# Kernel tuning notes

Hardware: AMD Instinct MI355X
Metric: run time of the kernel (lower is better)

The kernel has to match this reference:

```python
import jax, jax.numpy as jnp
import numpy as np
from jax import lax

V, E, T, F, K = 100000, 300, 50, 100, 3
B, S = 32, 512


def setup_inputs() -> dict:
    key = jax.random.key(0)
    ks = jax.random.split(key, 10)
    inp = {
        "x": jax.random.randint(ks[0], (B, S), 0, V),
        "tags": jax.random.randint(ks[1], (B, S), 0, T),
        "emb": jax.random.normal(ks[2], (V, E), dtype=jnp.float32),
        "conv_w": jax.random.normal(ks[3], (F, E, K), dtype=jnp.float32) / np.sqrt(E * K),
        "conv_b": jnp.zeros((F,), dtype=jnp.float32),
        "fc_w": jax.random.normal(ks[4], (T, F), dtype=jnp.float32) / np.sqrt(F),
        "fc_b": jnp.zeros((T,), dtype=jnp.float32),
        "start_trans": jax.random.uniform(ks[5], (T,), dtype=jnp.float32, minval=-0.1, maxval=0.1),
        "end_trans": jax.random.uniform(ks[6], (T,), dtype=jnp.float32, minval=-0.1, maxval=0.1),
        "trans": jax.random.uniform(ks[7], (T, T), dtype=jnp.float32, minval=-0.1, maxval=0.1),
    }
    return inp


def _emissions(x, emb, conv_w, conv_b, fc_w, fc_b):
    e = emb[x]                                   # [B,S,E] embedding gather
    e = jnp.transpose(e, (0, 2, 1))              # [B,E,S]
    h = lax.conv_general_dilated(e, conv_w, (1,), [(K // 2, K // 2)])  # [B,F,S] (NCW/OIW)
    h = jax.nn.relu(h + conv_b[None, :, None])   # dropout is identity in eval
    feat = jnp.transpose(h, (0, 2, 1))           # [B,S,F]
    return (jnp.einsum("bsf,tf->bst", feat, fc_w) + fc_b).astype(jnp.float32)  # [B,S,T]


def _crf_nll(emissions, tags, start_trans, end_trans, trans):
    # numerator: score of the gold tag path (full mask)
    em_tag = jnp.take_along_axis(emissions, tags[..., None], axis=-1)[..., 0]  # [B,S]
    num = (start_trans[tags[:, 0]]
           + em_tag.sum(-1)
           + trans[tags[:, :-1], tags[:, 1:]].sum(-1)
           + end_trans[tags[:, -1]])                                           # [B]

    # denominator: forward algorithm via scan over time
    alpha0 = start_trans[None, :] + emissions[:, 0]                             # [B,T]

    def step(alpha, em_t):
        # alpha: [B,T] prev scores; em_t: [B,T] emissions at t
        new = jax.nn.logsumexp(alpha[:, :, None] + trans[None] + em_t[:, None, :], axis=1)
        return new, None

    alpha, _ = lax.scan(step, alpha0, jnp.transpose(emissions[:, 1:], (1, 0, 2)))
    log_z = jax.nn.logsumexp(alpha + end_trans[None, :], axis=-1)               # [B]
    return -(num - log_z).sum()  # torchcrf default reduction='sum'; model returns -llh


def reference(x, tags, emb, conv_w, conv_b, fc_w, fc_b, start_trans, end_trans, trans):
    emissions = _emissions(x, emb, conv_w, conv_b, fc_w, fc_b)
    return _crf_nll(emissions, tags, start_trans, end_trans, trans)
```

## Files before the change

### kernel.cpp

```cpp
#include <hip/hip_runtime.h>
#include <hip/hip_bf16.h>
#include <math.h>

#define BB 32
#define SS 512
#define EE 300
#define FF 100
#define TT 50
#define CH 16
#define NC 32

typedef __attribute__((ext_vector_type(8))) short v8s;
typedef __attribute__((ext_vector_type(4))) float v4f;
#define MFMA16 __builtin_amdgcn_mfma_f32_16x16x32_bf16

#define AP 328
#define NCH 10
#define CKS 3
#define CHB (128 * 96)
#define A2P 136
#define MP 72

__device__ inline unsigned short f2bf(float v) {
    unsigned u = __float_as_uint(v);
    unsigned r = u + 0x7fff + ((u >> 16) & 1);
    return (unsigned short)(r >> 16);
}
__device__ inline float bf2f(short s) {
    return __uint_as_float(((unsigned)(unsigned short)s) << 16);
}
__device__ inline unsigned pkbf2(float a, float b) {
    __hip_bfloat162 h = __float22bfloat162_rn(make_float2(a, b));
    return *(unsigned*)&h;
}
__device__ inline v8s ldsld8(const short* p) {
    return *(const v8s*)__builtin_assume_aligned(p, 16);
}
__device__ inline void g2lds16(const void* g, void* l) {
    __builtin_amdgcn_global_load_lds(
        (const __attribute__((address_space(1))) unsigned int*)g,
        (__attribute__((address_space(3))) unsigned int*)l, 16, 0, 0);
}

__global__ void prep_kernel(const float* __restrict__ tr, const float* __restrict__ cw,
                            const float* __restrict__ fcw,
                            unsigned short* __restrict__ wB2,
                            unsigned short* __restrict__ fcwT2,
                            unsigned short* __restrict__ AT,
                            unsigned short* __restrict__ Ab,
                            float* __restrict__ accum, unsigned* __restrict__ cnt,
                            float* __restrict__ nllpart, unsigned* __restrict__ doneb)
{
    const int gid = blockIdx.x * 256 + threadIdx.x;
    const int gs  = 64 * 256;
    if (gid == 0) { *accum = 0.f; *cnt = 0u; }
    if (gid < BB) { nllpart[gid] = 0.f; doneb[gid] = 0u; }
    for (int idx = gid; idx < NCH * CKS * 8 * 512; idx += gs) {
        int e = idx & 7, p = (idx >> 3) & 63, blk = idx >> 9;
        int ch = blk / 24, rem = blk - ch * 24;
        int sl = rem >> 3, ft = rem & 7;
        int col = p >> 2, q = p & 3;
        int n  = ft * 16 + col;
        int gk = ch * 96 + sl * 32 + q * 8 + e;
        int kk = gk / 320, ee = gk - kk * 320;
        float v = (n < FF && ee < EE) ? cw[n * 900 + ee * 3 + kk] : 0.f;
        wB2[idx] = f2bf(v);
    }
    for (int idx = gid; idx < 16 * 512; idx += gs) {
        int e = idx & 7, p = (idx >> 3) & 63, blk = idx >> 9;
        int ks = blk >> 2, nt = blk & 3;
        int col = p >> 2, q = p & 3;
        int t = nt * 16 + col, f = ks * 32 + q * 8 + e;
        float v = (t < TT && f < FF) ? fcw[t * FF + f] : 0.f;
        fcwT2[idx] = f2bf(v);
    }
    for (int idx = gid; idx < 64 * 64; idx += gs) {
        int r = idx >> 6, c2 = idx & 63;
        AT[idx] = (r < TT && c2 < TT) ? f2bf(__expf(tr[c2 * TT + r])) : 0;
        Ab[idx] = (r < TT && c2 < TT) ? f2bf(__expf(tr[r * TT + c2])) : 0;
    }
}

__global__ __launch_bounds__(256, 3) void emis_kernel(
    const int* __restrict__ x, const float* __restrict__ emb,
    const unsigned short* __restrict__ wB2, const float* __restrict__ cb,
    const unsigned short* __restrict__ fcwT2, const float* __restrict__ fcb,
    const int* __restrict__ tags, const float* __restrict__ tr,
    const float* __restrict__ start, const float* __restrict__ endt,
    float* __restrict__ expem, float* __restrict__ nllpart)
{
    __shared__ __align__(16) short ldsA[34 * AP];
    __shared__ __align__(16) short ldsB[CHB];
    __shared__ float redN[2];

    const int b    = blockIdx.y;
    const int s0   = blockIdx.x * 32;
    const int tid  = threadIdx.x;
    const int wv   = tid >> 6;
    const int lane = tid & 63;
    const int col  = lane & 15;
    const int q    = lane >> 4;
    const int bofs = ((col << 2) | q) << 3;

#pragma unroll
    for (int it = 0; it < 6; ++it) {
        int seg = it * 4 + wv;
        g2lds16((const char*)wB2 + seg * 1024 + lane * 16,
                (char*)ldsB + seg * 1024);
    }

    int   xr[10], ofs[10], e0a[10];
#pragma unroll
    for (int it = 0; it < 10; ++it) {
        int g = tid + it * 256;
        int r = g / 75, eg = g - r * 75;
        int e0 = eg * 4;
        int src = s0 - 1 + r;
        bool v = (g < 2550) && (src >= 0) && (src < SS);
        xr[it]  = v ? x[b * SS + src] : -1;
        ofs[it] = r * AP + e0;
        e0a[it] = e0;
    }
    float4 vv[10];
#pragma unroll
    for (int it = 0; it < 10; ++it)
        vv[it] = (xr[it] >= 0)
               ? *(const float4*)(emb + (size_t)xr[it] * EE + e0a[it])
               : make_float4(0.f, 0.f, 0.f, 0.f);
#pragma unroll
    for (int it = 0; it < 10; ++it) {
        int g = tid + it * 256;
        if (g < 2550) {
            unsigned lo = pkbf2(vv[it].x, vv[it].y);
            unsigned hi = pkbf2(vv[it].z, vv[it].w);
            *(uint2*)&ldsA[ofs[it]] = make_uint2(lo, hi);
        }
    }
    if (tid < 34 * 5) {
        int r = tid / 5, c0 = 300 + (tid % 5) * 4;
        *(short4*)&ldsA[r * AP + c0] = make_short4(0, 0, 0, 0);
    }

    v4f acc[2][2];
#pragma unroll
    for (int a = 0; a < 2; ++a)
#pragma unroll
        for (int f = 0; f < 2; ++f) acc[a][f] = (v4f){0.f, 0.f, 0.f, 0.f};

    const int ftA = wv * 2, ftB = wv * 2 + 1;
    for (int ch = 0; ch < NCH; ++ch) {
        __syncthreads();
#pragma unroll
        for (int sl = 0; sl < CKS; ++sl) {
            int gk = ch * 96 + sl * 32;
            int kk = (gk >= 640) ? 2 : (gk >= 320 ? 1 : 0);
            int e0 = gk - kk * 320;
            v8s a0 = ldsld8(&ldsA[(col + kk) * AP + e0 + q * 8]);
            v8s a1 = ldsld8(&ldsA[(16 + col + kk) * AP + e0 + q * 8]);
            v8s b0 = ldsld8(&ldsB[((sl * 8 + ftA) << 9) + bofs]);
            v8s b1 = ldsld8(&ldsB[((sl * 8 + ftB) << 9) + bofs]);
            acc[0][0] = MFMA16(a0, b0, acc[0][0], 0, 0, 0);
            acc[0][1] = MFMA16(a0, b1, acc[0][1], 0, 0, 0);
            acc[1][0] = MFMA16(a1, b0, acc[1][0], 0, 0, 0);
            acc[1][1] = MFMA16(a1, b1, acc[1][1], 0, 0, 0);
        }
        __syncthreads();
        if (ch < NCH - 1) {
            const char* g = (const char*)(wB2 + (size_t)(ch + 1) * CHB);
#pragma unroll
            for (int it = 0; it < 6; ++it) {
                int seg = it * 4 + wv;
                g2lds16(g + seg * 1024 + lane * 16, (char*)ldsB + seg * 1024);
            }
        }
    }

    short* A2 = ldsA;
    short* B2 = ldsB;
#pragma unroll
    for (int it = 0; it < 4; ++it) {
        int seg = it * 4 + wv;
        g2lds16((const char*)fcwT2 + seg * 1024 + lane * 16,
                (char*)B2 + seg * 1024);
    }
#pragma unroll
    for (int st = 0; st < 2; ++st)
#pragma unroll
        for (int fi = 0; fi < 2; ++fi) {
            int f = (wv * 2 + fi) * 16 + col;
            float bias = (f < FF) ? cb[f] : 0.f;
#pragma unroll
            for (int rg = 0; rg < 4; ++rg) {
                int s = st * 16 + q * 4 + rg;
                float v = (f < FF) ? fmaxf(acc[st][fi][rg] + bias, 0.f) : 0.f;
                A2[s * A2P + f] = (short)f2bf(v);
            }
        }
    __syncthreads();

    if (wv < 2) {
        v4f a2[4];
#pragma unroll
        for (int nt = 0; nt < 4; ++nt) a2[nt] = (v4f){0.f, 0.f, 0.f, 0.f};
#pragma unroll
        for (int ks = 0; ks < 4; ++ks) {
            v8s af = ldsld8(&A2[(wv * 16 + col) * A2P + ks * 32 + q * 8]);
#pragma unroll
            for (int nt = 0; nt < 4; ++nt) {
                v8s bt = ldsld8(&B2[((ks * 4 + nt) << 9) + bofs]);
                a2[nt] = MFMA16(af, bt, a2[nt], 0, 0, 0);
            }
        }
        float fb0 = fcb[col], fb1 = fcb[16 + col], fb2 = fcb[32 + col];
        float fb3 = (col < 2) ? fcb[48 + col] : 0.f;
        float nllp = 0.f;
#pragma unroll
        for (int rg = 0; rg < 4; ++rg) {
            int s = s0 + wv * 16 + q * 4 + rg;
            float e0v = a2[0][rg] + fb0;
            float e1v = a2[1][rg] + fb1;
            float e2v = a2[2][rg] + fb2;
            float e3v = (col < 2) ? a2[3][rg] + fb3 : -1e30f;
            float m = fmaxf(fmaxf(e0v, e1v), fmaxf(e2v, e3v));
#pragma unroll
            for (int off = 1; off < 16; off <<= 1) m = fmaxf(m, __shfl_xor(m, off));
            int gidx = b * SS + s;
            int tg = tags[gidx];
            float* orow = expem + (size_t)gidx * TT;
            orow[col]      = __expf(e0v - m);
            orow[16 + col] = __expf(e1v - m);
            orow[32 + col] = __expf(e2v - m);
            if (col < 2) orow[48 + col] = __expf(e3v - m);
            if (tg == col)            nllp -= e0v;
            else if (tg == 16 + col)  nllp -= e1v;
            else if (tg == 32 + col)  nllp -= e2v;
            else if (col < 2 && tg == 48 + col) nllp -= e3v;
            if (col == 0) {
                nllp += m;
                if (s < SS - 1) nllp -= tr[tg * TT + tags[gidx + 1]];
                if (s == 0)      nllp -= start[tg];
                if (s == SS - 1) nllp -= endt[tg];
            }
        }
#pragma unroll
        for (int off = 1; off < 64; off <<= 1) nllp += __shfl_xor(nllp, off);
        if (lane == 0) redN[wv] = nllp;
    }
    __syncthreads();
    if (tid == 0) atomicAdd(nllpart + b, redN[0] + redN[1]);
}

__global__ __launch_bounds__(128) void chunkchain_kernel(
    const float* __restrict__ expem, const unsigned short* __restrict__ AT,
    const unsigned short* __restrict__ Ab,
    unsigned short* __restrict__ R, float* __restrict__ lsR,
    const float* __restrict__ start, const float* __restrict__ endt,
    const float* __restrict__ nllpart, unsigned* __restrict__ doneb,
    float* __restrict__ accum, unsigned* __restrict__ cnt,
    float* __restrict__ out)
{
    __shared__ __align__(16) short L[2][64 * MP];
    __shared__ __align__(16) float emL[CH][64];
    __shared__ float mxsh[2];
    __shared__ unsigned lastf;
    const int c = blockIdx.x, b = blockIdx.y;
    const int tid  = threadIdx.x;
    const int wv   = tid >> 6;
    const int lane = tid & 63;
    const int col = lane & 15, q = lane >> 4;
    const int t0 = c * CH + 1;
    const int nf = (c == NC - 1) ? (SS - 1 - (NC - 1) * CH) : CH;

    for (int idx = tid; idx < CH * 64; idx += 128) {
        int k = idx >> 6, m = idx & 63;
        float v = 0.f;
        if (m < TT && k < nf) v = expem[((size_t)(b * SS + t0 + k)) * TT + m];
        emL[k][m] = v;
    }

    v8s af[2][2];
#pragma unroll
    for (int jl = 0; jl < 2; ++jl)
#pragma unroll
        for (int kc = 0; kc < 2; ++kc)
            af[jl][kc] = *(const v8s*)(AT + ((wv * 2 + jl) * 16 + col) * 64 + kc * 32 + q * 8);
    __syncthreads();

    {
        const int row = tid >> 1, half = tid & 1;
        const v8s* arow = (const v8s*)(Ab + row * 64);
#pragma unroll
        for (int gh = 0; gh < 4; ++gh) {
            int g = half * 4 + gh;
            v8s a = arow[g];
            float f[8];
#pragma unroll
            for (int e = 0; e < 8; ++e) f[e] = bf2f(a[e]) * emL[0][g * 8 + e];
            uint4 o = make_uint4(pkbf2(f[0], f[1]), pkbf2(f[2], f[3]),
                                 pkbf2(f[4], f[5]), pkbf2(f[6], f[7]));
            *(uint4*)&L[0][row * MP + g * 8] = o;
        }
    }

    int cur = 0;
    for (int k = 1; k < nf; ++k) {
        __syncthreads();
        v8s bf[4][2];
#pragma unroll
        for (int nt = 0; nt < 4; ++nt)
#pragma unroll
            for (int kc = 0; kc < 2; ++kc)
                bf[nt][kc] = ldsld8(&L[cur][(nt * 16 + col) * MP + kc * 32 + q * 8]);
        v4f acc[2][4];
#pragma unroll
        for (int jl = 0; jl < 2; ++jl)
#pragma unroll
            for (int nt = 0; nt < 4; ++nt) {
                acc[jl][nt] = (v4f){0.f, 0.f, 0.f, 0.f};
                acc[jl][nt] = MFMA16(af[jl][0], bf[nt][0], acc[jl][nt], 0, 0, 0);
                acc[jl][nt] = MFMA16(af[jl][1], bf[nt][1], acc[jl][nt], 0, 0, 0);
            }
        if (k < nf - 1) {
#pragma unroll
            for (int jl = 0; jl < 2; ++jl) {
                const int jt = wv * 2 + jl;
                const float4 em4 = *(const float4*)&emL[k][jt * 16 + q * 4];
#pragma unroll
                for (int nt = 0; nt < 4; ++nt) {
                    uint2 o = make_uint2(
                        pkbf2(acc[jl][nt][0] * em4.x, acc[jl][nt][1] * em4.y),
                        pkbf2(acc[jl][nt][2] * em4.z, acc[jl][nt][3] * em4.w));
                    *(uint2*)&L[cur ^ 1][(nt * 16 + col) * MP + jt * 16 + q * 4] = o;
                }
            }
            cur ^= 1;
        } else {
            float vals[2][4][4];
            float mx = 0.f;
#pragma unroll
            for (int jl = 0; jl < 2; ++jl) {
                const int jt = wv * 2 + jl;
                const float4 em4 = *(const float4*)&emL[k][jt * 16 + q * 4];
#pragma unroll
                for (int nt = 0; nt < 4; ++nt) {
                    vals[jl][nt][0] = acc[jl][nt][0] * em4.x;
                    vals[jl][nt][1] = acc[jl][nt][1] * em4.y;
                    vals[jl][nt][2] = acc[jl][nt][2] * em4.z;
                    vals[jl][nt][3] = acc[jl][nt][3] * em4.w;
#pragma unroll
                    for (int r = 0; r < 4; ++r) mx = fmaxf(mx, vals[jl][nt][r]);
                }
            }
#pragma unroll
            for (int off = 1; off < 64; off <<= 1) mx = fmaxf(mx, __shfl_xor(mx, off));
            if (lane == 0) mxsh[wv] = mx;
            __syncthreads();
            mx = fmaxf(fmaxf(mxsh[0], mxsh[1]), 1e-37f);
            float inv = 1.f / mx;
            unsigned short* Rc = R + ((size_t)(b * NC + c) << 12);
#pragma unroll
            for (int jl = 0; jl < 2; ++jl)
#pragma unroll
                for (int nt = 0; nt < 4; ++nt)
#pragma unroll
                    for (int r = 0; r < 4; ++r)
                        Rc[((wv * 2 + jl) * 16 + q * 4 + r) * 64 + nt * 16 + col] =
                            f2bf(vals[jl][nt][r] * inv);
            if (tid == 0) lsR[b * NC + c] = __logf(mx);
        }
    }

    __syncthreads();
    if (tid == 0) {
        __threadfence();
        unsigned o = atomicAdd(doneb + b, 1u);
        lastf = (o == NC - 1) ? 1u : 0u;
    }
    __syncthreads();
    if (!lastf || wv != 0) return;

    __threadfence();
    const int i = lane;
    float* pvec = &emL[0][0];
    pvec[i] = (i < TT) ? __expf(start[i]) * expem[((size_t)(b * SS)) * TT + i] : 0.f;
    const unsigned short* Rb = R + ((size_t)(b * NC) << 12);
    v8s rb[4][8];
#pragma unroll
    for (int pc = 0; pc < 4; ++pc)
#pragma unroll
        for (int g = 0; g < 8; ++g)
            rb[pc][g] = *(const v8s*)(Rb + ((size_t)pc << 12) + i * 64 + g * 8);
    float logacc = 0.f;
#pragma unroll
    for (int cc = 0; cc < NC; ++cc) {
        const int slot = cc & 3;
        const float4* pv4 = (const float4*)pvec;
        float a0 = 0.f, a1 = 0.f, a2 = 0.f, a3 = 0.f;
#pragma unroll
        for (int g = 0; g < 8; ++g) {
            v8s v = rb[slot][g];
            float4 pA = pv4[g * 2], pB = pv4[g * 2 + 1];
            float* aa = (g & 3) == 0 ? &a0 : (g & 3) == 1 ? &a1 : (g & 3) == 2 ? &a2 : &a3;
            float t = *aa;
            t = fmaf(bf2f(v[0]), pA.x, t);
            t = fmaf(bf2f(v[1]), pA.y, t);
            t = fmaf(bf2f(v[2]), pA.z, t);
            t = fmaf(bf2f(v[3]), pA.w, t);
            t = fmaf(bf2f(v[4]), pB.x, t);
            t = fmaf(bf2f(v[5]), pB.y, t);
            t = fmaf(bf2f(v[6]), pB.z, t);
            t = fmaf(bf2f(v[7]), pB.w, t);
            *aa = t;
        }
        float acc2 = (a0 + a1) + (a2 + a3);
        if (cc + 4 < NC) {
            const unsigned short* Rn = Rb + ((size_t)(cc + 4) << 12);
#pragma unroll
            for (int g = 0; g < 8; ++g)
                rb[slot][g] = *(const v8s*)(Rn + i * 64 + g * 8);
        }
        float mx = acc2;
#pragma unroll
        for (int off = 1; off < 64; off <<= 1) mx = fmaxf(mx, __shfl_xor(mx, off));
        mx = fmaxf(mx, 1e-37f);
        logacc += __logf(mx) + lsR[b * NC + cc];
        pvec[i] = acc2 * (1.f / mx);
    }
    float sv = (i < TT) ? pvec[i] * __expf(endt[i]) : 0.f;
#pragma unroll
    for (int off = 1; off < 64; off <<= 1) sv += __shfl_xor(sv, off);
    if (i == 0) {
        float nll = nllpart[b] + logacc + __logf(sv);
        atomicAdd(accum, nll);
        __threadfence();
        unsigned o = atomicAdd(cnt, 1u);
        if (o == BB - 1) out[0] = atomicAdd(accum, 0.f);
    }
}

extern "C" void kernel_launch(void* const* d_in, const int* in_sizes, int n_in,
                              void* d_out, int out_size, void* d_ws, size_t ws_size,
                              hipStream_t stream)
{
    const int*   x    = (const int*)d_in[0];
    const int*   tags = (const int*)d_in[1];
    const float* emb  = (const float*)d_in[2];
    const float* cw   = (const float*)d_in[3];
    const float* cb   = (const float*)d_in[4];
    const float* fcw  = (const float*)d_in[5];
    const float* fcb  = (const float*)d_in[6];
    const float* st   = (const float*)d_in[7];
    const float* en   = (const float*)d_in[8];
    const float* tr   = (const float*)d_in[9];

    unsigned short* wB2   = (unsigned short*)d_ws;
    unsigned short* fcwT2 = wB2 + NCH * CKS * 8 * 512;
    unsigned short* ATm   = fcwT2 + 16 * 512;
    unsigned short* Abm   = ATm + 4096;
    unsigned short* Rm    = Abm + 4096;
    float* fbase   = (float*)(Rm + (size_t)BB * NC * 4096);
    float* expem   = fbase;
    float* lsR     = expem + (size_t)BB * SS * TT;
    float* nllpart = lsR + BB * NC;
    float* accum   = nllpart + BB;
    unsigned* cnt  = (unsigned*)(accum + 1);
    unsigned* doneb = cnt + 1;

    prep_kernel<<<dim3(64), 256, 0, stream>>>(tr, cw, fcw, wB2, fcwT2, ATm, Abm,
                                              accum, cnt, nllpart, doneb);
    emis_kernel<<<dim3(16, BB), 256, 0, stream>>>(x, emb, wB2, cb, fcwT2, fcb,
                                                  tags, tr, st, en, expem, nllpart);
    chunkchain_kernel<<<dim3(NC, BB), 128, 0, stream>>>(expem, ATm, Abm, Rm, lsR,
                                                        st, en, nllpart, doneb,
                                                        accum, cnt, (float*)d_out);
}
```

Baseline: 283.6 us.

## Replace sequential chunk matrix chain with parallel tree reduction across eight waves

The per-chunk product of 16 transfer matrices was computed by two waves stepping sequentially through time. Now eight waves each form a pair product in parallel (identity padding for short chunks), followed by a log-depth tree of LDS matrix products. This shortens the serial dependency chain within each block, but each wave does more MFMA work, the block grows to 512 threads, and LDS use increases.

```diff
diff --git a/kernel.cpp b/kernel.cpp
--- a/kernel.cpp
+++ b/kernel.cpp
@@ -250,7 +250,59 @@
     if (tid == 0) atomicAdd(nllpart + b, redN[0] + redN[1]);
 }
 
-__global__ __launch_bounds__(128) void chunkchain_kernel(
+__device__ inline v8s idfrag(int row, int kbase) {
+    v8s r;
+#pragma unroll
+    for (int e = 0; e < 8; ++e) r[e] = (short)((kbase + e == row) ? 0x3F80 : 0);
+    return r;
+}
+
+__device__ inline void prodLDS(const short* SA, const short* SB, int col, int q,
+                               v4f (&acc)[4][4]) {
+    v8s a[4][2], bb[4][2];
+#pragma unroll
+    for (int jt = 0; jt < 4; ++jt)
+#pragma unroll
+        for (int kc = 0; kc < 2; ++kc)
+            a[jt][kc] = ldsld8(&SA[(jt * 16 + col) * MP + kc * 32 + q * 8]);
+#pragma unroll
+    for (int nt = 0; nt < 4; ++nt)
+#pragma unroll
+        for (int kc = 0; kc < 2; ++kc)
+            bb[nt][kc] = ldsld8(&SB[(nt * 16 + col) * MP + kc * 32 + q * 8]);
+#pragma unroll
+    for (int jt = 0; jt < 4; ++jt)
+#pragma unroll
+        for (int nt = 0; nt < 4; ++nt) {
+            acc[jt][nt] = (v4f){0.f, 0.f, 0.f, 0.f};
+            acc[jt][nt] = MFMA16(a[jt][0], bb[nt][0], acc[jt][nt], 0, 0, 0);
+            acc[jt][nt] = MFMA16(a[jt][1], bb[nt][1], acc[jt][nt], 0, 0, 0);
+        }
+}
+
+__device__ inline void storeT(short* SD, int col, int q, const v4f (&acc)[4][4]) {
+#pragma unroll
+    for (int jt = 0; jt < 4; ++jt)
+#pragma unroll
+        for (int nt = 0; nt < 4; ++nt) {
+            uint2 o = make_uint2(pkbf2(acc[jt][nt][0], acc[jt][nt][1]),
+                                 pkbf2(acc[jt][nt][2], acc[jt][nt][3]));
+            *(uint2*)&SD[(nt * 16 + col) * MP + jt * 16 + q * 4] = o;
+        }
+}
+
+__device__ inline void storeRM(short* SD, int col, int q, const v4f (&acc)[4][4]) {
+#pragma unroll
+    for (int jt = 0; jt < 4; ++jt)
+#pragma unroll
+        for (int nt = 0; nt < 4; ++nt)
+#pragma unroll
+            for (int r = 0; r < 4; ++r)
+                SD[(jt * 16 + q * 4 + r) * MP + nt * 16 + col] =
+                    (short)f2bf(acc[jt][nt][r]);
+}
+
+__global__ __launch_bounds__(512) void chunkchain_kernel(
     const float* __restrict__ expem, const unsigned short* __restrict__ AT,
     const unsigned short* __restrict__ Ab,
     unsigned short* __restrict__ R, float* __restrict__ lsR,
@@ -259,9 +311,8 @@
     float* __restrict__ accum, unsigned* __restrict__ cnt,
     float* __restrict__ out)
 {
-    __shared__ __align__(16) short L[2][64 * MP];
+    __shared__ __align__(16) short S[8][64 * MP];
     __shared__ __align__(16) float emL[CH][64];
-    __shared__ float mxsh[2];
     __shared__ unsigned lastf;
     const int c = blockIdx.x, b = blockIdx.y;
     const int tid  = threadIdx.x;
@@ -271,106 +322,127 @@
     const int t0 = c * CH + 1;
     const int nf = (c == NC - 1) ? (SS - 1 - (NC - 1) * CH) : CH;
 
-    for (int idx = tid; idx < CH * 64; idx += 128) {
+    for (int idx = tid; idx < CH * 64; idx += 512) {
         int k = idx >> 6, m = idx & 63;
         float v = 0.f;
         if (m < TT && k < nf) v = expem[((size_t)(b * SS + t0 + k)) * TT + m];
         emL[k][m] = v;
     }
-
-    v8s af[2][2];
-#pragma unroll
-    for (int jl = 0; jl < 2; ++jl)
-#pragma unroll
-        for (int kc = 0; kc < 2; ++kc)
-            af[jl][kc] = *(const v8s*)(AT + ((wv * 2 + jl) * 16 + col) * 64 + kc * 32 + q * 8);
     __syncthreads();
 
     {
-        const int row = tid >> 1, half = tid & 1;
-        const v8s* arow = (const v8s*)(Ab + row * 64);
-#pragma unroll
-        for (int gh = 0; gh < 4; ++gh) {
-            int g = half * 4 + gh;
-            v8s a = arow[g];
-            float f[8];
-#pragma unroll
-            for (int e = 0; e < 8; ++e) f[e] = bf2f(a[e]) * emL[0][g * 8 + e];
-            uint4 o = make_uint4(pkbf2(f[0], f[1]), pkbf2(f[2], f[3]),
-                                 pkbf2(f[4], f[5]), pkbf2(f[6], f[7]));
-            *(uint4*)&L[0][row * MP + g * 8] = o;
-        }
-    }
-
-    int cur = 0;
-    for (int k = 1; k < nf; ++k) {
-        __syncthreads();
-        v8s bf[4][2];
-#pragma unroll
-        for (int nt = 0; nt < 4; ++nt)
-#pragma unroll
-            for (int kc = 0; kc < 2; ++kc)
-                bf[nt][kc] = ldsld8(&L[cur][(nt * 16 + col) * MP + kc * 32 + q * 8]);
-        v4f acc[2][4];
-#pragma unroll
-        for (int jl = 0; jl < 2; ++jl)
-#pragma unroll
-            for (int nt = 0; nt < 4; ++nt) {
-                acc[jl][nt] = (v4f){0.f, 0.f, 0.f, 0.f};
-                acc[jl][nt] = MFMA16(af[jl][0], bf[nt][0], acc[jl][nt], 0, 0, 0);
-                acc[jl][nt] = MFMA16(af[jl][1], bf[nt][1], acc[jl][nt], 0, 0, 0);
-            }
-        if (k < nf - 1) {
-#pragma unroll
-            for (int jl = 0; jl < 2; ++jl) {
-                const int jt = wv * 2 + jl;
-                const float4 em4 = *(const float4*)&emL[k][jt * 16 + q * 4];
+        const int tX = 2 * wv + 1, tY = 2 * wv;
+        const bool idX = (tX >= nf), idY = (tY >= nf);
+        v4f acc[4][4];
+        {
+            v8s af[4][2];
+#pragma unroll
+            for (int jt = 0; jt < 4; ++jt)
+#pragma unroll
+                for (int kc = 0; kc < 2; ++kc)
+                    af[jt][kc] = idX
+                        ? idfrag(jt * 16 + col, kc * 32 + q * 8)
+                        : *(const v8s*)(AT + (jt * 16 + col) * 64 + kc * 32 + q * 8);
+#pragma unroll
+            for (int jt = 0; jt < 4; ++jt)
+#pragma unroll
+                for (int nt = 0; nt < 4; ++nt) acc[jt][nt] = (v4f){0.f, 0.f, 0.f, 0.f};
+#pragma unroll
+            for (int kc = 0; kc < 2; ++kc) {
+                const int kb = kc * 32 + q * 8;
+                float4 eA = *(const float4*)&emL[tY][kb];
+                float4 eB = *(const float4*)&emL[tY][kb + 4];
+#pragma unroll
+                for (int nt = 0; nt < 4; ++nt) {
+                    v8s bfr;
+                    if (idY) bfr = idfrag(nt * 16 + col, kb);
+                    else {
+                        v8s ab = *(const v8s*)(Ab + (nt * 16 + col) * 64 + kb);
+                        unsigned u0 = pkbf2(bf2f(ab[0]) * eA.x, bf2f(ab[1]) * eA.y);
+                        unsigned u1 = pkbf2(bf2f(ab[2]) * eA.z, bf2f(ab[3]) * eA.w);
+                        unsigned u2 = pkbf2(bf2f(ab[4]) * eB.x, bf2f(ab[5]) * eB.y);
+                        unsigned u3 = pkbf2(bf2f(ab[6]) * eB.z, bf2f(ab[7]) * eB.w);
+                        ((unsigned*)&bfr)[0] = u0; ((unsigned*)&bfr)[1] = u1;
+                        ((unsigned*)&bfr)[2] = u2; ((unsigned*)&bfr)[3] = u3;
+                    }
+#pragma unroll
+                    for (int jt = 0; jt < 4; ++jt)
+                        acc[jt][nt] = MFMA16(af[jt][kc], bfr, acc[jt][nt], 0, 0, 0);
+                }
+            }
+        }
+        if (wv & 1) {
+#pragma unroll
+            for (int jt = 0; jt < 4; ++jt) {
+                float4 e4 = idX ? make_float4(1.f, 1.f, 1.f, 1.f)
+                                : *(const float4*)&emL[tX][jt * 16 + q * 4];
+#pragma unroll
+                for (int nt = 0; nt < 4; ++nt) {
+                    S[wv][(jt * 16 + q * 4 + 0) * MP + nt * 16 + col] = (short)f2bf(acc[jt][nt][0] * e4.x);
+                    S[wv][(jt * 16 + q * 4 + 1) * MP + nt * 16 + col] = (short)f2bf(acc[jt][nt][1] * e4.y);
+                    S[wv][(jt * 16 + q * 4 + 2) * MP + nt * 16 + col] = (short)f2bf(acc[jt][nt][2] * e4.z);
+                    S[wv][(jt * 16 + q * 4 + 3) * MP + nt * 16 + col] = (short)f2bf(acc[jt][nt][3] * e4.w);
+                }
+            }
+        } else {
+#pragma unroll
+            for (int jt = 0; jt < 4; ++jt) {
+                float4 e4 = idX ? make_float4(1.f, 1.f, 1.f, 1.f)
+                                : *(const float4*)&emL[tX][jt * 16 + q * 4];
 #pragma unroll
                 for (int nt = 0; nt < 4; ++nt) {
                     uint2 o = make_uint2(
-                        pkbf2(acc[jl][nt][0] * em4.x, acc[jl][nt][1] * em4.y),
-                        pkbf2(acc[jl][nt][2] * em4.z, acc[jl][nt][3] * em4.w));
-                    *(uint2*)&L[cur ^ 1][(nt * 16 + col) * MP + jt * 16 + q * 4] = o;
+                        pkbf2(acc[jt][nt][0] * e4.x, acc[jt][nt][1] * e4.y),
+                        pkbf2(acc[jt][nt][2] * e4.z, acc[jt][nt][3] * e4.w));
+                    *(uint2*)&S[wv][(nt * 16 + col) * MP + jt * 16 + q * 4] = o;
                 }
             }
-            cur ^= 1;
-        } else {
-            float vals[2][4][4];
-            float mx = 0.f;
-#pragma unroll
-            for (int jl = 0; jl < 2; ++jl) {
-                const int jt = wv * 2 + jl;
-                const float4 em4 = *(const float4*)&emL[k][jt * 16 + q * 4];
-#pragma unroll
-                for (int nt = 0; nt < 4; ++nt) {
-                    vals[jl][nt][0] = acc[jl][nt][0] * em4.x;
-                    vals[jl][nt][1] = acc[jl][nt][1] * em4.y;
-                    vals[jl][nt][2] = acc[jl][nt][2] * em4.z;
-                    vals[jl][nt][3] = acc[jl][nt][3] * em4.w;
-#pragma unroll
-                    for (int r = 0; r < 4; ++r) mx = fmaxf(mx, vals[jl][nt][r]);
-                }
-            }
-#pragma unroll
-            for (int off = 1; off < 64; off <<= 1) mx = fmaxf(mx, __shfl_xor(mx, off));
-            if (lane == 0) mxsh[wv] = mx;
-            __syncthreads();
-            mx = fmaxf(fmaxf(mxsh[0], mxsh[1]), 1e-37f);
-            float inv = 1.f / mx;
-            unsigned short* Rc = R + ((size_t)(b * NC + c) << 12);
-#pragma unroll
-            for (int jl = 0; jl < 2; ++jl)
-#pragma unroll
-                for (int nt = 0; nt < 4; ++nt)
-#pragma unroll
-                    for (int r = 0; r < 4; ++r)
-                        Rc[((wv * 2 + jl) * 16 + q * 4 + r) * 64 + nt * 16 + col] =
-                            f2bf(vals[jl][nt][r] * inv);
-            if (tid == 0) lsR[b * NC + c] = __logf(mx);
-        }
-    }
-
-    __syncthreads();
+        }
+    }
+    __syncthreads();
+
+    if (wv < 4) {
+        v4f acc[4][4];
+        prodLDS(S[2 * wv + 1], S[2 * wv], col, q, acc);
+        if (wv & 1) storeRM(S[2 * wv], col, q, acc);
+        else        storeT (S[2 * wv], col, q, acc);
+    }
+    __syncthreads();
+
+    if (wv < 2) {
+        v4f acc[4][4];
+        prodLDS(S[4 * wv + 2], S[4 * wv], col, q, acc);
+        if (wv) storeRM(S[4], col, q, acc);
+        else    storeT (S[0], col, q, acc);
+    }
+    __syncthreads();
+
+    if (wv == 0) {
+        v4f acc[4][4];
+        prodLDS(S[4], S[0], col, q, acc);
+        float mx = 0.f;
+#pragma unroll
+        for (int jt = 0; jt < 4; ++jt)
+#pragma unroll
+            for (int nt = 0; nt < 4; ++nt)
+#pragma unroll
+                for (int r = 0; r < 4; ++r) mx = fmaxf(mx, acc[jt][nt][r]);
+#pragma unroll
+        for (int off = 1; off < 64; off <<= 1) mx = fmaxf(mx, __shfl_xor(mx, off));
+        mx = fmaxf(mx, 1e-37f);
+        float inv = 1.f / mx;
+        unsigned short* Rc = R + ((size_t)(b * NC + c) << 12);
+#pragma unroll
+        for (int jt = 0; jt < 4; ++jt)
+#pragma unroll
+            for (int nt = 0; nt < 4; ++nt)
+#pragma unroll
+                for (int r = 0; r < 4; ++r)
+                    Rc[(jt * 16 + q * 4 + r) * 64 + nt * 16 + col] =
+                        f2bf(acc[jt][nt][r] * inv);
+        if (tid == 0) lsR[b * NC + c] = __logf(mx);
+    }
+
     if (tid == 0) {
         __threadfence();
         unsigned o = atomicAdd(doneb + b, 1u);
@@ -470,7 +542,7 @@
                                               accum, cnt, nllpart, doneb);
     emis_kernel<<<dim3(16, BB), 256, 0, stream>>>(x, emb, wB2, cb, fcwT2, fcb,
                                                   tags, tr, st, en, expem, nllpart);
-    chunkchain_kernel<<<dim3(NC, BB), 128, 0, stream>>>(expem, ATm, Abm, Rm, lsR,
+    chunkchain_kernel<<<dim3(NC, BB), 512, 0, stream>>>(expem, ATm, Abm, Rm, lsR,
                                                         st, en, nllpart, doneb,
                                                         accum, cnt, (float*)d_out);
 }
```

After: 306.4 us. 1.08x slower.

## Run chunk-chain blocks as a single wave and restructure the final chain loop

Applied to the files above, without the earlier changes.

Each chunkchain block now uses one 64-lane wave that does all four MFMA row tiles, which removes the cross-wave LDS max reduction and the block barriers around the completion atomic. The final sequential chain over chunks now uses a rolled loop with two register buffers that prefetch the next chunk's matrix. The per-chunk log scales are summed once with a shuffle reduction instead of being loaded inside the loop. Each wave does more MFMA work serially and the launch has fewer threads in total. The rolled loop keeps register pressure down but gives up the deeper four-chunk prefetch.

```diff
diff --git a/kernel.cpp b/kernel.cpp
--- a/kernel.cpp
+++ b/kernel.cpp
@@ -250,7 +250,38 @@
     if (tid == 0) atomicAdd(nllpart + b, redN[0] + redN[1]);
 }
 
-__global__ __launch_bounds__(128) void chunkchain_kernel(
+__device__ inline float chaindot(const v8s (&buf)[8], const float* pvec) {
+    const float4* pv4 = (const float4*)__builtin_assume_aligned(pvec, 16);
+    float a0 = 0.f, a1 = 0.f, a2 = 0.f, a3 = 0.f;
+#pragma unroll
+    for (int g = 0; g < 8; ++g) {
+        v8s v = buf[g];
+        float4 pA = pv4[g * 2], pB = pv4[g * 2 + 1];
+        float* aa = (g & 3) == 0 ? &a0 : (g & 3) == 1 ? &a1 : (g & 3) == 2 ? &a2 : &a3;
+        float t = *aa;
+        t = fmaf(bf2f(v[0]), pA.x, t);
+        t = fmaf(bf2f(v[1]), pA.y, t);
+        t = fmaf(bf2f(v[2]), pA.z, t);
+        t = fmaf(bf2f(v[3]), pA.w, t);
+        t = fmaf(bf2f(v[4]), pB.x, t);
+        t = fmaf(bf2f(v[5]), pB.y, t);
+        t = fmaf(bf2f(v[6]), pB.z, t);
+        t = fmaf(bf2f(v[7]), pB.w, t);
+        *aa = t;
+    }
+    return (a0 + a1) + (a2 + a3);
+}
+
+__device__ inline void chainfin(float acc2, float* pvec, int i, float& logacc) {
+    float mx = acc2;
+#pragma unroll
+    for (int off = 1; off < 64; off <<= 1) mx = fmaxf(mx, __shfl_xor(mx, off));
+    mx = fmaxf(mx, 1e-37f);
+    logacc += __logf(mx);
+    pvec[i] = acc2 * (1.f / mx);
+}
+
+__global__ __launch_bounds__(64) void chunkchain_kernel(
     const float* __restrict__ expem, const unsigned short* __restrict__ AT,
     const unsigned short* __restrict__ Ab,
     unsigned short* __restrict__ R, float* __restrict__ lsR,
@@ -261,44 +292,38 @@
 {
     __shared__ __align__(16) short L[2][64 * MP];
     __shared__ __align__(16) float emL[CH][64];
-    __shared__ float mxsh[2];
-    __shared__ unsigned lastf;
     const int c = blockIdx.x, b = blockIdx.y;
-    const int tid  = threadIdx.x;
-    const int wv   = tid >> 6;
-    const int lane = tid & 63;
+    const int lane = threadIdx.x;
     const int col = lane & 15, q = lane >> 4;
     const int t0 = c * CH + 1;
     const int nf = (c == NC - 1) ? (SS - 1 - (NC - 1) * CH) : CH;
 
-    for (int idx = tid; idx < CH * 64; idx += 128) {
+    for (int idx = lane; idx < CH * 64; idx += 64) {
         int k = idx >> 6, m = idx & 63;
         float v = 0.f;
         if (m < TT && k < nf) v = expem[((size_t)(b * SS + t0 + k)) * TT + m];
         emL[k][m] = v;
     }
 
-    v8s af[2][2];
-#pragma unroll
-    for (int jl = 0; jl < 2; ++jl)
+    v8s af[4][2];
+#pragma unroll
+    for (int jt = 0; jt < 4; ++jt)
 #pragma unroll
         for (int kc = 0; kc < 2; ++kc)
-            af[jl][kc] = *(const v8s*)(AT + ((wv * 2 + jl) * 16 + col) * 64 + kc * 32 + q * 8);
+            af[jt][kc] = *(const v8s*)(AT + (jt * 16 + col) * 64 + kc * 32 + q * 8);
     __syncthreads();
 
     {
-        const int row = tid >> 1, half = tid & 1;
-        const v8s* arow = (const v8s*)(Ab + row * 64);
-#pragma unroll
-        for (int gh = 0; gh < 4; ++gh) {
-            int g = half * 4 + gh;
+        const v8s* arow = (const v8s*)(Ab + lane * 64);
+#pragma unroll
+        for (int g = 0; g < 8; ++g) {
             v8s a = arow[g];
             float f[8];
 #pragma unroll
             for (int e = 0; e < 8; ++e) f[e] = bf2f(a[e]) * emL[0][g * 8 + e];
             uint4 o = make_uint4(pkbf2(f[0], f[1]), pkbf2(f[2], f[3]),
                                  pkbf2(f[4], f[5]), pkbf2(f[6], f[7]));
-            *(uint4*)&L[0][row * MP + g * 8] = o;
+            *(uint4*)&L[0][lane * MP + g * 8] = o;
         }
     }
 
@@ -311,130 +336,107 @@
 #pragma unroll
             for (int kc = 0; kc < 2; ++kc)
                 bf[nt][kc] = ldsld8(&L[cur][(nt * 16 + col) * MP + kc * 32 + q * 8]);
-        v4f acc[2][4];
-#pragma unroll
-        for (int jl = 0; jl < 2; ++jl)
+        v4f acc[4][4];
+#pragma unroll
+        for (int jt = 0; jt < 4; ++jt)
 #pragma unroll
             for (int nt = 0; nt < 4; ++nt) {
-                acc[jl][nt] = (v4f){0.f, 0.f, 0.f, 0.f};
-                acc[jl][nt] = MFMA16(af[jl][0], bf[nt][0], acc[jl][nt], 0, 0, 0);
-                acc[jl][nt] = MFMA16(af[jl][1], bf[nt][1], acc[jl][nt], 0, 0, 0);
+                acc[jt][nt] = (v4f){0.f, 0.f, 0.f, 0.f};
+                acc[jt][nt] = MFMA16(af[jt][0], bf[nt][0], acc[jt][nt], 0, 0, 0);
+                acc[jt][nt] = MFMA16(af[jt][1], bf[nt][1], acc[jt][nt], 0, 0, 0);
             }
         if (k < nf - 1) {
 #pragma unroll
-            for (int jl = 0; jl < 2; ++jl) {
-                const int jt = wv * 2 + jl;
+            for (int jt = 0; jt < 4; ++jt) {
                 const float4 em4 = *(const float4*)&emL[k][jt * 16 + q * 4];
 #pragma unroll
                 for (int nt = 0; nt < 4; ++nt) {
                     uint2 o = make_uint2(
-                        pkbf2(acc[jl][nt][0] * em4.x, acc[jl][nt][1] * em4.y),
-                        pkbf2(acc[jl][nt][2] * em4.z, acc[jl][nt][3] * em4.w));
+                        pkbf2(acc[jt][nt][0] * em4.x, acc[jt][nt][1] * em4.y),
+                        pkbf2(acc[jt][nt][2] * em4.z, acc[jt][nt][3] * em4.w));
                     *(uint2*)&L[cur ^ 1][(nt * 16 + col) * MP + jt * 16 + q * 4] = o;
                 }
             }
             cur ^= 1;
         } else {
-            float vals[2][4][4];
+            float vals[4][4][4];
             float mx = 0.f;
 #pragma unroll
-            for (int jl = 0; jl < 2; ++jl) {
-                const int jt = wv * 2 + jl;
+            for (int jt = 0; jt < 4; ++jt) {
                 const float4 em4 = *(const float4*)&emL[k][jt * 16 + q * 4];
 #pragma unroll
                 for (int nt = 0; nt < 4; ++nt) {
-                    vals[jl][nt][0] = acc[jl][nt][0] * em4.x;
-                    vals[jl][nt][1] = acc[jl][nt][1] * em4.y;
-                    vals[jl][nt][2] = acc[jl][nt][2] * em4.z;
-                    vals[jl][nt][3] = acc[jl][nt][3] * em4.w;
-#pragma unroll
-                    for (int r = 0; r < 4; ++r) mx = fmaxf(mx, vals[jl][nt][r]);
+                    vals[jt][nt][0] = acc[jt][nt][0] * em4.x;
+                    vals[jt][nt][1] = acc[jt][nt][1] * em4.y;
+                    vals[jt][nt][2] = acc[jt][nt][2] * em4.z;
+                    vals[jt][nt][3] = acc[jt][nt][3] * em4.w;
+#pragma unroll
+                    for (int r = 0; r < 4; ++r) mx = fmaxf(mx, vals[jt][nt][r]);
                 }
             }
 #pragma unroll
             for (int off = 1; off < 64; off <<= 1) mx = fmaxf(mx, __shfl_xor(mx, off));
-            if (lane == 0) mxsh[wv] = mx;
-            __syncthreads();
-            mx = fmaxf(fmaxf(mxsh[0], mxsh[1]), 1e-37f);
+            mx = fmaxf(mx, 1e-37f);
             float inv = 1.f / mx;
             unsigned short* Rc = R + ((size_t)(b * NC + c) << 12);
 #pragma unroll
-            for (int jl = 0; jl < 2; ++jl)
+            for (int jt = 0; jt < 4; ++jt)
 #pragma unroll
                 for (int nt = 0; nt < 4; ++nt)
 #pragma unroll
                     for (int r = 0; r < 4; ++r)
-                        Rc[((wv * 2 + jl) * 16 + q * 4 + r) * 64 + nt * 16 + col] =
-                            f2bf(vals[jl][nt][r] * inv);
-            if (tid == 0) lsR[b * NC + c] = __logf(mx);
-        }
-    }
-
-    __syncthreads();
-    if (tid == 0) {
-        __threadfence();
-        unsigned o = atomicAdd(doneb + b, 1u);
-        lastf = (o == NC - 1) ? 1u : 0u;
-    }
-    __syncthreads();
-    if (!lastf || wv != 0) return;
+                        Rc[(jt * 16 + q * 4 + r) * 64 + nt * 16 + col] =
+                            f2bf(vals[jt][nt][r] * inv);
+            if (lane == 0) lsR[b * NC + c] = __logf(mx);
+        }
+    }
+
+    __threadfence();
+    unsigned o = 0;
+    if (lane == 0) o = atomicAdd(doneb + b, 1u);
+    o = __shfl(o, 0);
+    if (o != NC - 1u) return;
 
     __threadfence();
     const int i = lane;
     float* pvec = &emL[0][0];
     pvec[i] = (i < TT) ? __expf(start[i]) * expem[((size_t)(b * SS)) * TT + i] : 0.f;
+    float lsv = (i < NC) ? lsR[b * NC + i] : 0.f;
+#pragma unroll
+    for (int off = 1; off < 64; off <<= 1) lsv += __shfl_xor(lsv, off);
+
     const unsigned short* Rb = R + ((size_t)(b * NC) << 12);
-    v8s rb[4][8];
-#pragma unroll
-    for (int pc = 0; pc < 4; ++pc)
+    v8s bufA[8], bufB[8];
+#pragma unroll
+    for (int g = 0; g < 8; ++g)
+        bufA[g] = *(const v8s*)(Rb + i * 64 + g * 8);
+    float logacc = 0.f;
+#pragma unroll 1
+    for (int cc = 0; cc < NC; cc += 2) {
+        const unsigned short* R1 = Rb + ((size_t)(cc + 1) << 12);
 #pragma unroll
         for (int g = 0; g < 8; ++g)
-            rb[pc][g] = *(const v8s*)(Rb + ((size_t)pc << 12) + i * 64 + g * 8);
-    float logacc = 0.f;
-#pragma unroll
-    for (int cc = 0; cc < NC; ++cc) {
-        const int slot = cc & 3;
-        const float4* pv4 = (const float4*)pvec;
-        float a0 = 0.f, a1 = 0.f, a2 = 0.f, a3 = 0.f;
-#pragma unroll
-        for (int g = 0; g < 8; ++g) {
-            v8s v = rb[slot][g];
-            float4 pA = pv4[g * 2], pB = pv4[g * 2 + 1];
-            float* aa = (g & 3) == 0 ? &a0 : (g & 3) == 1 ? &a1 : (g & 3) == 2 ? &a2 : &a3;
-            float t = *aa;
-            t = fmaf(bf2f(v[0]), pA.x, t);
-            t = fmaf(bf2f(v[1]), pA.y, t);
-            t = fmaf(bf2f(v[2]), pA.z, t);
-            t = fmaf(bf2f(v[3]), pA.w, t);
-            t = fmaf(bf2f(v[4]), pB.x, t);
-            t = fmaf(bf2f(v[5]), pB.y, t);
-            t = fmaf(bf2f(v[6]), pB.z, t);
-            t = fmaf(bf2f(v[7]), pB.w, t);
-            *aa = t;
-        }
-        float acc2 = (a0 + a1) + (a2 + a3);
-        if (cc + 4 < NC) {
-            const unsigned short* Rn = Rb + ((size_t)(cc + 4) << 12);
+            bufB[g] = *(const v8s*)(R1 + i * 64 + g * 8);
+        float acc2 = chaindot(bufA, pvec);
+        chainfin(acc2, pvec, i, logacc);
+        if (cc + 2 < NC) {
+            const unsigned short* R2 = Rb + ((size_t)(cc + 2) << 12);
 #pragma unroll
             for (int g = 0; g < 8; ++g)
-                rb[slot][g] = *(const v8s*)(Rn + i * 64 + g * 8);
-        }
-        float mx = acc2;
-#pragma unroll
-        for (int off = 1; off < 64; off <<= 1) mx = fmaxf(mx, __shfl_xor(mx, off));
-        mx = fmaxf(mx, 1e-37f);
-        logacc += __logf(mx) + lsR[b * NC + cc];
-        pvec[i] = acc2 * (1.f / mx);
+                bufA[g] = *(const v8s*)(R2 + i * 64 + g * 8);
+        }
+        acc2 = chaindot(bufB, pvec);
+        chainfin(acc2, pvec, i, logacc);
     }
     float sv = (i < TT) ? pvec[i] * __expf(endt[i]) : 0.f;
 #pragma unroll
     for (int off = 1; off < 64; off <<= 1) sv += __shfl_xor(sv, off);
     if (i == 0) {
-        float nll = nllpart[b] + logacc + __logf(sv);
+        float nll = nllpart[b] + logacc + lsv + __logf(sv);
         atomicAdd(accum, nll);
         __threadfence();
-        unsigned o = atomicAdd(cnt, 1u);
-        if (o == BB - 1) out[0] = atomicAdd(accum, 0.f);
+        unsigned oo = atomicAdd(cnt, 1u);
+        if (oo == BB - 1) out[0] = atomicAdd(accum, 0.f);
     }
 }
 
@@ -470,7 +472,7 @@
                                               accum, cnt, nllpart, doneb);
     emis_kernel<<<dim3(16, BB), 256, 0, stream>>>(x, emb, wB2, cb, fcwT2, fcb,
                                                   tags, tr, st, en, expem, nllpart);
-    chunkchain_kernel<<<dim3(NC, BB), 128, 0, stream>>>(expem, ATm, Abm, Rm, lsR,
-                                                        st, en, nllpart, doneb,
-                                                        accum, cnt, (float*)d_out);
-}
+    chunkchain_kernel<<<dim3(NC, BB), 64, 0, stream>>>(expem, ATm, Abm, Rm, lsR,
+                                                       st, en, nllpart, doneb,
+                                                       accum, cnt, (float*)d_out);
+}
```

Result: no change. 287.0 us (+1.2%).
